# Optimization experiments

Measured on AMD Instinct MI355X. Metric: run time of the kernel, lower is better.

Reference implementation:

```python
import jax, jax.numpy as jnp
import numpy as np

D_MODEL = 1024
N_HEADS = 16
D_K = D_MODEL // N_HEADS
FF_DIM = 4096
EPS = 1e-6
NEG = -1.0e9


def _layernorm(x, g, b):
    # torch: a_2 * (x - mean) / (std + eps) + b_2, std is unbiased (ddof=1)
    mean = jnp.mean(x, axis=-1, keepdims=True)
    std = jnp.std(x, axis=-1, keepdims=True, ddof=1)
    return g * (x - mean) / (std + EPS) + b


def setup_inputs() -> dict:
    key = jax.random.key(0)
    ks = jax.random.split(key, 8)
    s = 0.02
    x = jax.random.normal(ks[0], (2, 2048, D_MODEL), dtype=jnp.float32)
    mask = jnp.ones((2, 1, 1, 2048), dtype=jnp.int32)
    return {
        "x": x,
        "mask": mask,
        "wq": jax.random.normal(ks[1], (D_MODEL, D_MODEL), jnp.float32) * s,
        "wk": jax.random.normal(ks[2], (D_MODEL, D_MODEL), jnp.float32) * s,
        "wv": jax.random.normal(ks[3], (D_MODEL, D_MODEL), jnp.float32) * s,
        "wo": jax.random.normal(ks[4], (D_MODEL, D_MODEL), jnp.float32) * s,
        "bq": jnp.zeros((D_MODEL,), jnp.float32),
        "bk": jnp.zeros((D_MODEL,), jnp.float32),
        "bv": jnp.zeros((D_MODEL,), jnp.float32),
        "bo": jnp.zeros((D_MODEL,), jnp.float32),
        "w1": jax.random.normal(ks[5], (D_MODEL, FF_DIM), jnp.float32) * s,
        "b1": jnp.zeros((FF_DIM,), jnp.float32),
        "w2": jax.random.normal(ks[6], (FF_DIM, D_MODEL), jnp.float32) * s,
        "b2": jnp.zeros((D_MODEL,), jnp.float32),
        "ln1_g": jnp.ones((D_MODEL,), jnp.float32),
        "ln1_b": jnp.zeros((D_MODEL,), jnp.float32),
        "ln2_g": jnp.ones((D_MODEL,), jnp.float32),
        "ln2_b": jnp.zeros((D_MODEL,), jnp.float32),
    }


def reference(x, mask, wq, wk, wv, wo, bq, bk, bv, bo, w1, b1, w2, b2,
              ln1_g, ln1_b, ln2_g, ln2_b):
    B, S, _ = x.shape
    # --- sublayer 1: pre-norm self-attention with residual ---
    h = _layernorm(x, ln1_g, ln1_b)
    q = (h @ wq + bq).reshape(B, S, N_HEADS, D_K).transpose(0, 2, 1, 3)
    k = (h @ wk + bk).reshape(B, S, N_HEADS, D_K).transpose(0, 2, 1, 3)
    v = (h @ wv + bv).reshape(B, S, N_HEADS, D_K).transpose(0, 2, 1, 3)
    scores = jnp.einsum('bhqd,bhkd->bhqk', q, k) / np.sqrt(D_K).astype(np.float32)
    scores = jnp.where(mask == 0, NEG, scores)
    attn = jax.nn.softmax(scores, axis=-1)
    ctx = jnp.einsum('bhqk,bhkd->bhqd', attn, v)
    ctx = ctx.transpose(0, 2, 1, 3).reshape(B, S, D_MODEL)
    x = x + (ctx @ wo + bo)
    # --- sublayer 2: pre-norm FFN with residual ---
    h2 = _layernorm(x, ln2_g, ln2_b)
    ff = jax.nn.relu(h2 @ w1 + b1) @ w2 + b2
    return x + ff
```

## Files before the change

### kernel.cpp

```cpp
#include <hip/hip_runtime.h>

typedef unsigned short u16;
typedef unsigned int u32;
typedef __attribute__((ext_vector_type(8))) short bf16x8;
typedef __attribute__((ext_vector_type(4))) float f32x4;

__device__ __forceinline__ u16 f2bf(float f) {
  union { float f; unsigned int u; } x;
  x.f = f;
  unsigned int r = x.u + 0x7fffu + ((x.u >> 16) & 1u);
  return (u16)(r >> 16);
}

__device__ __forceinline__ float bf2f(u16 v) {
  union { unsigned int u; float f; } x;
  x.u = ((unsigned int)v) << 16;
  return x.f;
}

__device__ __forceinline__ u32 fbits(float f) {
  union { float f; u32 u; } x; x.f = f; return x.u;
}

__device__ __forceinline__ void async16(const u16* g, u16* l) {
  __builtin_amdgcn_global_load_lds((const __attribute__((address_space(1))) void*)g,
                                   (__attribute__((address_space(3))) void*)l, 16, 0, 0);
}

__device__ __forceinline__ void stage128x64(const u16* __restrict__ src, long row0, int k0,
                                            int ld, u16* lds, int wave, int lane) {
#pragma unroll
  for (int r = 0; r < 4; ++r) {
    int s = r * 256 + wave * 64 + lane;
    int row = s >> 3;
    int c = (s & 7) ^ (row & 7);
    async16(src + (row0 + row) * (long)ld + k0 + c * 8, lds + (r * 256 + wave * 64) * 8);
  }
}

__device__ __forceinline__ void stage64x128(const u16* __restrict__ src, int col0, int ld,
                                            u16* lds, int wave, int lane) {
#pragma unroll
  for (int r = 0; r < 4; ++r) {
    int s = r * 256 + wave * 64 + lane;
    int row = s >> 4;
    int c = (s & 15) ^ (row & 15);
    async16(src + (long)row * ld + col0 + c * 8, lds + (r * 256 + wave * 64) * 8);
  }
}

__global__ __launch_bounds__(256) void transpose_cvt(const float* __restrict__ src,
                                                     u16* __restrict__ dst, int R, int C) {
  __shared__ float tile[32][33];
  int c0 = blockIdx.x * 32, r0 = blockIdx.y * 32;
  int tx = threadIdx.x & 31, ty = threadIdx.x >> 5;
#pragma unroll
  for (int i = 0; i < 32; i += 8)
    tile[ty + i][tx] = src[(long)(r0 + ty + i) * C + c0 + tx];
  __syncthreads();
#pragma unroll
  for (int i = 0; i < 32; i += 8)
    dst[(long)(c0 + ty + i) * R + r0 + tx] = f2bf(tile[tx][ty + i]);
}

__global__ __launch_bounds__(256) void transpose_cvt4(const float* __restrict__ s0,
                                                      const float* __restrict__ s1,
                                                      const float* __restrict__ s2,
                                                      const float* __restrict__ s3,
                                                      u16* __restrict__ dst) {
  __shared__ float tile[32][33];
  const float* src = blockIdx.z == 0 ? s0 : (blockIdx.z == 1 ? s1 : (blockIdx.z == 2 ? s2 : s3));
  u16* d = dst + (long)blockIdx.z * 1024 * 1024;
  int c0 = blockIdx.x * 32, r0 = blockIdx.y * 32;
  int tx = threadIdx.x & 31, ty = threadIdx.x >> 5;
#pragma unroll
  for (int i = 0; i < 32; i += 8)
    tile[ty + i][tx] = src[(long)(r0 + ty + i) * 1024 + c0 + tx];
  __syncthreads();
#pragma unroll
  for (int i = 0; i < 32; i += 8)
    d[(long)(c0 + ty + i) * 1024 + r0 + tx] = f2bf(tile[tx][ty + i]);
}

__device__ __forceinline__ void ln_core(float4 v, const float* g, const float* b, int t,
                                        u16* outrow) {
  float s = v.x + v.y + v.z + v.w;
  float ss = v.x * v.x + v.y * v.y + v.z * v.z + v.w * v.w;
#pragma unroll
  for (int off = 32; off; off >>= 1) {
    s += __shfl_xor(s, off);
    ss += __shfl_xor(ss, off);
  }
  __shared__ float red[8];
  int wave = t >> 6, lane = t & 63;
  if (lane == 0) { red[wave] = s; red[wave + 4] = ss; }
  __syncthreads();
  float tot = red[0] + red[1] + red[2] + red[3];
  float tots = red[4] + red[5] + red[6] + red[7];
  float mean = tot * (1.0f / 1024.0f);
  float var = (tots - 1024.0f * mean * mean) * (1.0f / 1023.0f);
  var = fmaxf(var, 0.0f);
  float inv = 1.0f / (sqrtf(var) + 1e-6f);
  float4 gv = ((const float4*)g)[t];
  float4 bv = ((const float4*)b)[t];
  union { unsigned long long u64; u16 h[4]; } o;
  o.h[0] = f2bf(gv.x * (v.x - mean) * inv + bv.x);
  o.h[1] = f2bf(gv.y * (v.y - mean) * inv + bv.y);
  o.h[2] = f2bf(gv.z * (v.z - mean) * inv + bv.z);
  o.h[3] = f2bf(gv.w * (v.w - mean) * inv + bv.w);
  *(unsigned long long*)(outrow + t * 4) = o.u64;
}

__global__ __launch_bounds__(256) void layernorm_rows(const float* __restrict__ x,
                                                      const float* __restrict__ g,
                                                      const float* __restrict__ b,
                                                      u16* __restrict__ out) {
  int row = blockIdx.x, t = threadIdx.x;
  float4 v = ((const float4*)(x + (long)row * 1024))[t];
  ln_core(v, g, b, t, out + (long)row * 1024);
}

__global__ __launch_bounds__(256) void ln_fuse(const float* __restrict__ x,
                                               const float* __restrict__ bres,
                                               const u16* __restrict__ p0,
                                               const u16* __restrict__ p1,
                                               const float* __restrict__ g,
                                               const float* __restrict__ b,
                                               float* __restrict__ yout,
                                               u16* __restrict__ hout) {
  int row = blockIdx.x, t = threadIdx.x;
  long base = (long)row * 1024;
  float4 xv = ((const float4*)(x + base))[t];
  float4 bo = ((const float4*)bres)[t];
  ushort4 a = ((const ushort4*)(p0 + base))[t];
  ushort4 c = ((const ushort4*)(p1 + base))[t];
  float4 y;
  y.x = xv.x + bo.x + bf2f(a.x) + bf2f(c.x);
  y.y = xv.y + bo.y + bf2f(a.y) + bf2f(c.y);
  y.z = xv.z + bo.z + bf2f(a.z) + bf2f(c.z);
  y.w = xv.w + bo.w + bf2f(a.w) + bf2f(c.w);
  ((float4*)(yout + base))[t] = y;
  ln_core(y, g, b, t, hout + base);
}

__global__ __launch_bounds__(256) void final_add(float* __restrict__ out,
                                                 const float* __restrict__ b2,
                                                 const u16* __restrict__ p0,
                                                 const u16* __restrict__ p1) {
  int row = blockIdx.x, t = threadIdx.x;
  long base = (long)row * 1024;
  float4 o = ((float4*)(out + base))[t];
  float4 bb = ((const float4*)b2)[t];
  ushort4 a = ((const ushort4*)(p0 + base))[t];
  ushort4 c = ((const ushort4*)(p1 + base))[t];
  o.x += bb.x + bf2f(a.x) + bf2f(c.x);
  o.y += bb.y + bf2f(a.y) + bf2f(c.y);
  o.z += bb.z + bf2f(a.z) + bf2f(c.z);
  o.w += bb.w + bf2f(a.w) + bf2f(c.w);
  ((float4*)(out + base))[t] = o;
}

template <int MODE>
__global__ __launch_bounds__(256) void gemm_bt(const u16* __restrict__ A,
                                               const u16* __restrict__ Bt, int M, int N, int K,
                                               void* __restrict__ outp,
                                               const float* __restrict__ bias0,
                                               const float* __restrict__ bias1,
                                               const float* __restrict__ bias2,
                                               u16* __restrict__ q_out, u16* __restrict__ k_out,
                                               u16* __restrict__ v_out) {
  __shared__ __align__(16) u16 lds[17408];
  u16* ldsA = lds;
  u16* ldsB = lds + 8192;
  const int tid = threadIdx.x;
  const int wave = tid >> 6, lane = tid & 63;
  const int lane16 = lane & 15, quad = lane >> 4;
  const int wm = (wave >> 1) * 64, wn = (wave & 1) * 64;
  const long m0 = (long)blockIdx.y * 128;
  const long n0 = (long)blockIdx.x * 128;
  const int kLen = K / gridDim.z;
  const int kBeg = blockIdx.z * kLen;

  const f32x4 fzero = {0.f, 0.f, 0.f, 0.f};
  f32x4 acc[4][4];
#pragma unroll
  for (int i = 0; i < 4; ++i)
#pragma unroll
    for (int j = 0; j < 4; ++j) acc[i][j] = fzero;

  for (int k0 = kBeg; k0 < kBeg + kLen; k0 += 64) {
    stage128x64(A, m0, k0, K, ldsA, wave, lane);
    stage128x64(Bt, n0, k0, K, ldsB, wave, lane);
    __syncthreads();
#pragma unroll
    for (int kk = 0; kk < 2; ++kk) {
      bf16x8 af[4], bfr[4];
#pragma unroll
      for (int i = 0; i < 4; ++i) {
        int row = wm + i * 16 + lane16;
        int c = (kk * 4 + quad) ^ (row & 7);
        af[i] = *(const bf16x8*)(ldsA + row * 64 + c * 8);
      }
#pragma unroll
      for (int j = 0; j < 4; ++j) {
        int row = wn + j * 16 + lane16;
        int c = (kk * 4 + quad) ^ (row & 7);
        bfr[j] = *(const bf16x8*)(ldsB + row * 64 + c * 8);
      }
#pragma unroll
      for (int i = 0; i < 4; ++i)
#pragma unroll
        for (int j = 0; j < 4; ++j)
          acc[i][j] = __builtin_amdgcn_mfma_f32_16x16x32_bf16(af[i], bfr[j], acc[i][j], 0, 0, 0);
    }
    __syncthreads();
  }

  if (MODE == 0 && (int)(n0 >> 10) == 2) {
#pragma unroll
    for (int j = 0; j < 4; ++j) {
      int lcol = wn + j * 16 + lane16;
      float bvj = bias2[(int)(n0 - 2048) + lcol];
#pragma unroll
      for (int i = 0; i < 4; ++i)
#pragma unroll
        for (int r = 0; r < 4; ++r) {
          int lrow = wm + i * 16 + quad * 4 + r;
          lds[lcol * 136 + lrow] = f2bf(acc[i][j][r] + bvj);
        }
    }
    __syncthreads();
    int lcol = tid >> 1, seg = tid & 1;
    int cc = (int)(n0 - 2048) + lcol;
    int head = cc >> 6, d = cc & 63;
    int bI = (int)(m0 >> 11), s0 = (int)(m0 & 2047);
    u16* dst = v_out + ((long)(bI * 16 + head) * 64 + d) * 2048 + s0 + seg * 64;
    const u16* s = lds + lcol * 136 + seg * 64;
#pragma unroll
    for (int c2 = 0; c2 < 8; ++c2) ((uint4*)dst)[c2] = ((const uint4*)s)[c2];
    return;
  }

  u16* pp = nullptr;
  if (MODE == 1) {
    pp = blockIdx.z == 0 ? (u16*)outp : (blockIdx.z == 1 ? q_out : (blockIdx.z == 2 ? k_out : v_out));
  }

#pragma unroll
  for (int j = 0; j < 4; ++j) {
    int col = (int)n0 + wn + j * 16 + lane16;
#pragma unroll
    for (int i = 0; i < 4; ++i) {
#pragma unroll
      for (int r = 0; r < 4; ++r) {
        int row = (int)m0 + wm + i * 16 + quad * 4 + r;
        float val = acc[i][j][r];
        if (MODE == 0) {
          int which = col >> 10, cc = col & 1023;
          float vv = val + (which == 0 ? bias0[cc] : bias1[cc]);
          int bb = row >> 11, sS = row & 2047, head = cc >> 6, d = cc & 63;
          long bh = (long)bb * 16 + head;
          if (which == 0) {
            q_out[(bh * 2048 + sS) * 64 + d] = f2bf(vv * 0.18033688f);
          } else {
            k_out[(bh * 2048 + sS) * 64 + d] = f2bf(vv);
          }
        } else if (MODE == 1) {
          pp[(long)row * N + col] = f2bf(val);
        } else if (MODE == 2) {
          ((u16*)outp)[(long)row * N + col] = f2bf(fmaxf(val + bias0[col], 0.0f));
        }
      }
    }
  }
}

#define FA_C0 28.854239f
__global__ __launch_bounds__(256) void flash_attn(const u16* __restrict__ q,
                                                  const u16* __restrict__ k,
                                                  const u16* __restrict__ v,
                                                  const int* __restrict__ mask,
                                                  u16* __restrict__ ctx) {
  const int bh = blockIdx.y;
  const int b = bh >> 4, h = bh & 15;
  const int q0 = blockIdx.x * 128;
  const int tid = threadIdx.x;
  const int wave = tid >> 6, lane = tid & 63;
  const int lane16 = lane & 15, quad = lane >> 4;

  const u16* qp = q + (long)bh * 2048 * 64;
  const u16* kp = k + (long)bh * 2048 * 64;
  const u16* vp = v + (long)bh * 64 * 2048;
  const int* mp = mask + b * 2048;

  __shared__ __align__(16) u16 ldsK[128 * 64];
  __shared__ __align__(16) u16 ldsVT[64 * 128];
  __shared__ __align__(16) u16 ldsP23[2 * 4096];
  __shared__ __align__(16) float ldsMask[128];
  __shared__ int ldsFlag[2];
  u16* myP = (wave < 2) ? (ldsK + wave * 4096) : (ldsP23 + (wave - 2) * 4096);

  bf16x8 qf[2][2];
#pragma unroll
  for (int g = 0; g < 2; ++g) {
    const long qrow = q0 + wave * 32 + g * 16 + lane16;
    qf[g][0] = *(const bf16x8*)(qp + qrow * 64 + quad * 8);
    qf[g][1] = *(const bf16x8*)(qp + qrow * 64 + 32 + quad * 8);
  }

  const f32x4 fzero = {0.f, 0.f, 0.f, 0.f};
  const f32x4 cC0 = {-FA_C0, -FA_C0, -FA_C0, -FA_C0};
  float l_loc[2] = {0.f, 0.f};
  f32x4 o_acc[2][4];
#pragma unroll
  for (int g = 0; g < 2; ++g)
#pragma unroll
    for (int j = 0; j < 4; ++j) o_acc[g][j] = fzero;

  const int xorm = (lane16 & 7) << 2;

  for (int kt = 0; kt < 2048; kt += 128) {
    stage128x64(kp, kt, 0, 64, ldsK, wave, lane);
    stage64x128(vp, kt, 2048, ldsVT, wave, lane);
    if (tid < 128) {
      int mv = mp[kt + tid];
      ldsMask[tid] = ((mv == 0) ? -1.0e9f : 0.0f) - FA_C0;
      unsigned long long bal = __ballot(mv != 0);
      if ((tid & 63) == 0) ldsFlag[tid >> 6] = (bal == ~0ull) ? 1 : 0;
    }
    __syncthreads();
    const bool allv = (ldsFlag[0] & ldsFlag[1]) != 0;

    f32x4 s_acc[8][2];
#pragma unroll
    for (int j = 0; j < 8; ++j) {
      f32x4 ci = allv ? cC0 : *(const f32x4*)(ldsMask + j * 16 + quad * 4);
      int row = j * 16 + lane16;
      int c0i = quad ^ (row & 7);
      int c1i = (4 + quad) ^ (row & 7);
      bf16x8 kf0 = *(const bf16x8*)(ldsK + row * 64 + c0i * 8);
      bf16x8 kf1 = *(const bf16x8*)(ldsK + row * 64 + c1i * 8);
#pragma unroll
      for (int g = 0; g < 2; ++g) {
        f32x4 sa = __builtin_amdgcn_mfma_f32_16x16x32_bf16(kf0, qf[g][0], ci, 0, 0, 0);
        sa = __builtin_amdgcn_mfma_f32_16x16x32_bf16(kf1, qf[g][1], sa, 0, 0, 0);
        s_acc[j][g] = sa;
      }
    }
    __syncthreads();

#pragma unroll
    for (int j = 0; j < 8; ++j) {
      int cw = (4 * j + quad) ^ xorm;
#pragma unroll
      for (int g = 0; g < 2; ++g) {
        float p0 = __builtin_exp2f(s_acc[j][g][0]);
        float p1 = __builtin_exp2f(s_acc[j][g][1]);
        float p2 = __builtin_exp2f(s_acc[j][g][2]);
        float p3 = __builtin_exp2f(s_acc[j][g][3]);
        l_loc[g] += (p0 + p1) + (p2 + p3);
        u32 lo = __builtin_amdgcn_perm(fbits(p1), fbits(p0), 0x07060302u);
        u32 hi = __builtin_amdgcn_perm(fbits(p3), fbits(p2), 0x07060302u);
        uint2 pk; pk.x = lo; pk.y = hi;
        *(uint2*)(myP + (g * 16 + lane16) * 128 + cw * 4) = pk;
      }
    }
#pragma unroll
    for (int kk = 0; kk < 4; ++kk) {
      int cr = (8 * kk + 2 * quad) ^ xorm;
      bf16x8 pf0 = *(const bf16x8*)(myP + lane16 * 128 + cr * 4);
      bf16x8 pf1 = *(const bf16x8*)(myP + (16 + lane16) * 128 + cr * 4);
#pragma unroll
      for (int jj = 0; jj < 4; ++jj) {
        int row = jj * 16 + lane16;
        int cv = (kk * 4 + quad) ^ (row & 15);
        bf16x8 vf = *(const bf16x8*)(ldsVT + row * 128 + cv * 8);
        o_acc[0][jj] = __builtin_amdgcn_mfma_f32_16x16x32_bf16(pf0, vf, o_acc[0][jj], 0, 0, 0);
        o_acc[1][jj] = __builtin_amdgcn_mfma_f32_16x16x32_bf16(pf1, vf, o_acc[1][jj], 0, 0, 0);
      }
    }
    __syncthreads();
  }

  float lr[2][4];
#pragma unroll
  for (int g = 0; g < 2; ++g) {
    float l = l_loc[g];
#pragma unroll
    for (int off = 16; off < 64; off <<= 1) l += __shfl_xor(l, off);
    float linv = 1.0f / l;
#pragma unroll
    for (int r = 0; r < 4; ++r) lr[g][r] = __shfl(linv, quad * 4 + r);
  }

#pragma unroll
  for (int g = 0; g < 2; ++g)
#pragma unroll
    for (int jj = 0; jj < 4; ++jj)
#pragma unroll
      for (int r = 0; r < 4; ++r) {
        int sg = q0 + wave * 32 + g * 16 + quad * 4 + r;
        int d = jj * 16 + lane16;
        float val = o_acc[g][jj][r] * lr[g][r];
        ctx[((long)b * 2048 + sg) * 1024 + h * 64 + d] = f2bf(val);
      }
}

extern "C" void kernel_launch(void* const* d_in, const int* in_sizes, int n_in, void* d_out,
                              int out_size, void* d_ws, size_t ws_size, hipStream_t stream) {
  (void)in_sizes; (void)n_in; (void)out_size; (void)ws_size;
  const float* x  = (const float*)d_in[0];
  const int* mask = (const int*)d_in[1];
  const float* wq = (const float*)d_in[2];
  const float* wk = (const float*)d_in[3];
  const float* wv = (const float*)d_in[4];
  const float* wo = (const float*)d_in[5];
  const float* bq = (const float*)d_in[6];
  const float* bk = (const float*)d_in[7];
  const float* bv = (const float*)d_in[8];
  const float* bo = (const float*)d_in[9];
  const float* w1 = (const float*)d_in[10];
  const float* b1 = (const float*)d_in[11];
  const float* w2 = (const float*)d_in[12];
  const float* b2 = (const float*)d_in[13];
  const float* ln1_g = (const float*)d_in[14];
  const float* ln1_b = (const float*)d_in[15];
  const float* ln2_g = (const float*)d_in[16];
  const float* ln2_b = (const float*)d_in[17];
  float* out = (float*)d_out;

  u16* ws = (u16*)d_ws;
  u16* wqkvT = ws;
  u16* woT = wqkvT + 3072 * 1024;
  u16* w1T = woT + 1024 * 1024;
  u16* w2T = w1T + 4096 * 1024;
  u16* h   = w2T + 4096 * 1024;
  u16* qb  = h + 4096 * 1024;
  u16* kb  = qb + 4096 * 1024;
  u16* vb  = kb + 4096 * 1024;
  u16* ctx = vb + 4096 * 1024;
  u16* ffh = qb;
  u16* f2p0 = ws;
  u16* f2p1 = w1T;

  transpose_cvt4<<<dim3(32, 32, 4), 256, 0, stream>>>(wq, wk, wv, wo, wqkvT);
  transpose_cvt<<<dim3(128, 32), 256, 0, stream>>>(w1, w1T, 1024, 4096);
  transpose_cvt<<<dim3(32, 128), 256, 0, stream>>>(w2, w2T, 4096, 1024);

  layernorm_rows<<<4096, 256, 0, stream>>>(x, ln1_g, ln1_b, h);

  gemm_bt<0><<<dim3(24, 32), 256, 0, stream>>>(h, wqkvT, 4096, 3072, 1024, nullptr, bq, bk, bv,
                                               qb, kb, vb);

  flash_attn<<<dim3(16, 32), 256, 0, stream>>>(qb, kb, vb, mask, ctx);

  gemm_bt<1><<<dim3(8, 32, 2), 256, 0, stream>>>(ctx, woT, 4096, 1024, 1024, qb, nullptr,
                                                 nullptr, nullptr, kb, nullptr, nullptr);

  ln_fuse<<<4096, 256, 0, stream>>>(x, bo, qb, kb, ln2_g, ln2_b, out, h);

  gemm_bt<2><<<dim3(32, 32), 256, 0, stream>>>(h, w1T, 4096, 4096, 1024, ffh, b1, nullptr,
                                               nullptr, nullptr, nullptr, nullptr);

  gemm_bt<1><<<dim3(8, 32, 2), 256, 0, stream>>>(ffh, w2T, 4096, 1024, 4096, f2p0, nullptr,
                                                 nullptr, nullptr, f2p1, nullptr, nullptr);

  final_add<<<4096, 256, 0, stream>>>(out, b2, f2p0, f2p1);
}
```

Baseline: 376.7 us.

## Merge weight prep and layernorm into one launch; fuse softmax into QK loop

The three weight transpose/convert kernels and the first layernorm are folded into a single prep kernel that dispatches on block index, so four launches become one and their tails can overlap. In flash attention, P now has a dedicated LDS buffer per wave instead of reusing the K buffer for two waves. That lets exp2 and the P write happen straight after each QK MFMA without the intermediate score array or the extra barrier. The mask add is applied only when a tile is not fully valid, and the end-of-loop barrier moves to the start of the next iteration. The cost is more LDS per block, which may lower occupancy, and the mask offset constant is now always folded into the MFMA initial accumulator.

```diff
diff --git a/kernel.cpp b/kernel.cpp
--- a/kernel.cpp
+++ b/kernel.cpp
@@ -47,39 +47,6 @@
     int c = (s & 15) ^ (row & 15);
     async16(src + (long)row * ld + col0 + c * 8, lds + (r * 256 + wave * 64) * 8);
   }
-}
-
-__global__ __launch_bounds__(256) void transpose_cvt(const float* __restrict__ src,
-                                                     u16* __restrict__ dst, int R, int C) {
-  __shared__ float tile[32][33];
-  int c0 = blockIdx.x * 32, r0 = blockIdx.y * 32;
-  int tx = threadIdx.x & 31, ty = threadIdx.x >> 5;
-#pragma unroll
-  for (int i = 0; i < 32; i += 8)
-    tile[ty + i][tx] = src[(long)(r0 + ty + i) * C + c0 + tx];
-  __syncthreads();
-#pragma unroll
-  for (int i = 0; i < 32; i += 8)
-    dst[(long)(c0 + ty + i) * R + r0 + tx] = f2bf(tile[tx][ty + i]);
-}
-
-__global__ __launch_bounds__(256) void transpose_cvt4(const float* __restrict__ s0,
-                                                      const float* __restrict__ s1,
-                                                      const float* __restrict__ s2,
-                                                      const float* __restrict__ s3,
-                                                      u16* __restrict__ dst) {
-  __shared__ float tile[32][33];
-  const float* src = blockIdx.z == 0 ? s0 : (blockIdx.z == 1 ? s1 : (blockIdx.z == 2 ? s2 : s3));
-  u16* d = dst + (long)blockIdx.z * 1024 * 1024;
-  int c0 = blockIdx.x * 32, r0 = blockIdx.y * 32;
-  int tx = threadIdx.x & 31, ty = threadIdx.x >> 5;
-#pragma unroll
-  for (int i = 0; i < 32; i += 8)
-    tile[ty + i][tx] = src[(long)(r0 + ty + i) * 1024 + c0 + tx];
-  __syncthreads();
-#pragma unroll
-  for (int i = 0; i < 32; i += 8)
-    d[(long)(c0 + ty + i) * 1024 + r0 + tx] = f2bf(tile[tx][ty + i]);
 }
 
 __device__ __forceinline__ void ln_core(float4 v, const float* g, const float* b, int t,
@@ -111,13 +78,49 @@
   *(unsigned long long*)(outrow + t * 4) = o.u64;
 }
 
-__global__ __launch_bounds__(256) void layernorm_rows(const float* __restrict__ x,
-                                                      const float* __restrict__ g,
-                                                      const float* __restrict__ b,
-                                                      u16* __restrict__ out) {
-  int row = blockIdx.x, t = threadIdx.x;
-  float4 v = ((const float4*)(x + (long)row * 1024))[t];
-  ln_core(v, g, b, t, out + (long)row * 1024);
+__global__ __launch_bounds__(256) void prep(const float* __restrict__ wq,
+                                            const float* __restrict__ wk,
+                                            const float* __restrict__ wv,
+                                            const float* __restrict__ wo,
+                                            const float* __restrict__ w1,
+                                            const float* __restrict__ w2,
+                                            const float* __restrict__ x,
+                                            const float* __restrict__ ln1_g,
+                                            const float* __restrict__ ln1_b,
+                                            u16* __restrict__ wqkvT,
+                                            u16* __restrict__ w1T,
+                                            u16* __restrict__ w2T,
+                                            u16* __restrict__ hout) {
+  const int bid = blockIdx.x;
+  const int part = bid >> 12;
+  const int local = bid & 4095;
+  const int t = threadIdx.x;
+  if (part == 1) {
+    float4 v = ((const float4*)(x + (long)local * 1024))[t];
+    ln_core(v, ln1_g, ln1_b, t, hout + (long)local * 1024);
+    return;
+  }
+  __shared__ float tile[32][33];
+  const float* src; u16* dst; int C, R, bx, by;
+  if (part == 0) {
+    int sub = local >> 10;
+    src = sub == 0 ? wq : (sub == 1 ? wk : (sub == 2 ? wv : wo));
+    dst = wqkvT + (long)sub * 1024 * 1024;
+    C = 1024; R = 1024; bx = local & 31; by = (local >> 5) & 31;
+  } else if (part == 2) {
+    src = w1; dst = w1T; C = 4096; R = 1024; bx = local & 127; by = local >> 7;
+  } else {
+    src = w2; dst = w2T; C = 1024; R = 4096; bx = local & 31; by = local >> 5;
+  }
+  int c0 = bx * 32, r0 = by * 32;
+  int tx = t & 31, ty = t >> 5;
+#pragma unroll
+  for (int i = 0; i < 32; i += 8)
+    tile[ty + i][tx] = src[(long)(r0 + ty + i) * C + c0 + tx];
+  __syncthreads();
+#pragma unroll
+  for (int i = 0; i < 32; i += 8)
+    dst[(long)(c0 + ty + i) * R + r0 + tx] = f2bf(tile[tx][ty + i]);
 }
 
 __global__ __launch_bounds__(256) void ln_fuse(const float* __restrict__ x,
@@ -242,9 +245,7 @@
   }
 
   u16* pp = nullptr;
-  if (MODE == 1) {
-    pp = blockIdx.z == 0 ? (u16*)outp : (blockIdx.z == 1 ? q_out : (blockIdx.z == 2 ? k_out : v_out));
-  }
+  if (MODE == 1) pp = blockIdx.z == 0 ? (u16*)outp : q_out;
 
 #pragma unroll
   for (int j = 0; j < 4; ++j) {
@@ -295,10 +296,10 @@
 
   __shared__ __align__(16) u16 ldsK[128 * 64];
   __shared__ __align__(16) u16 ldsVT[64 * 128];
-  __shared__ __align__(16) u16 ldsP23[2 * 4096];
+  __shared__ __align__(16) u16 ldsP[4 * 4096];
   __shared__ __align__(16) float ldsMask[128];
   __shared__ int ldsFlag[2];
-  u16* myP = (wave < 2) ? (ldsK + wave * 4096) : (ldsP23 + (wave - 2) * 4096);
+  u16* myP = ldsP + wave * 4096;
 
   bf16x8 qf[2][2];
 #pragma unroll
@@ -318,58 +319,54 @@
     for (int j = 0; j < 4; ++j) o_acc[g][j] = fzero;
 
   const int xorm = (lane16 & 7) << 2;
+  u16* const pw0 = myP + lane16 * 128;
+  u16* const pw1 = myP + (16 + lane16) * 128;
 
   for (int kt = 0; kt < 2048; kt += 128) {
+    if (kt) __syncthreads();
     stage128x64(kp, kt, 0, 64, ldsK, wave, lane);
     stage64x128(vp, kt, 2048, ldsVT, wave, lane);
     if (tid < 128) {
       int mv = mp[kt + tid];
-      ldsMask[tid] = ((mv == 0) ? -1.0e9f : 0.0f) - FA_C0;
+      ldsMask[tid] = (mv == 0) ? -1.0e9f : 0.0f;
       unsigned long long bal = __ballot(mv != 0);
       if ((tid & 63) == 0) ldsFlag[tid >> 6] = (bal == ~0ull) ? 1 : 0;
     }
     __syncthreads();
     const bool allv = (ldsFlag[0] & ldsFlag[1]) != 0;
 
-    f32x4 s_acc[8][2];
 #pragma unroll
     for (int j = 0; j < 8; ++j) {
-      f32x4 ci = allv ? cC0 : *(const f32x4*)(ldsMask + j * 16 + quad * 4);
       int row = j * 16 + lane16;
       int c0i = quad ^ (row & 7);
       int c1i = (4 + quad) ^ (row & 7);
       bf16x8 kf0 = *(const bf16x8*)(ldsK + row * 64 + c0i * 8);
       bf16x8 kf1 = *(const bf16x8*)(ldsK + row * 64 + c1i * 8);
+      int cw = ((4 * j + quad) ^ xorm) * 4;
 #pragma unroll
       for (int g = 0; g < 2; ++g) {
-        f32x4 sa = __builtin_amdgcn_mfma_f32_16x16x32_bf16(kf0, qf[g][0], ci, 0, 0, 0);
+        f32x4 sa = __builtin_amdgcn_mfma_f32_16x16x32_bf16(kf0, qf[g][0], cC0, 0, 0, 0);
         sa = __builtin_amdgcn_mfma_f32_16x16x32_bf16(kf1, qf[g][1], sa, 0, 0, 0);
-        s_acc[j][g] = sa;
-      }
-    }
-    __syncthreads();
-
-#pragma unroll
-    for (int j = 0; j < 8; ++j) {
-      int cw = (4 * j + quad) ^ xorm;
-#pragma unroll
-      for (int g = 0; g < 2; ++g) {
-        float p0 = __builtin_exp2f(s_acc[j][g][0]);
-        float p1 = __builtin_exp2f(s_acc[j][g][1]);
-        float p2 = __builtin_exp2f(s_acc[j][g][2]);
-        float p3 = __builtin_exp2f(s_acc[j][g][3]);
+        if (!allv) {
+          f32x4 mk = *(const f32x4*)(ldsMask + j * 16 + quad * 4);
+          sa = sa + mk;
+        }
+        float p0 = __builtin_exp2f(sa[0]);
+        float p1 = __builtin_exp2f(sa[1]);
+        float p2 = __builtin_exp2f(sa[2]);
+        float p3 = __builtin_exp2f(sa[3]);
         l_loc[g] += (p0 + p1) + (p2 + p3);
-        u32 lo = __builtin_amdgcn_perm(fbits(p1), fbits(p0), 0x07060302u);
-        u32 hi = __builtin_amdgcn_perm(fbits(p3), fbits(p2), 0x07060302u);
-        uint2 pk; pk.x = lo; pk.y = hi;
-        *(uint2*)(myP + (g * 16 + lane16) * 128 + cw * 4) = pk;
+        uint2 pk;
+        pk.x = __builtin_amdgcn_perm(fbits(p1), fbits(p0), 0x07060302u);
+        pk.y = __builtin_amdgcn_perm(fbits(p3), fbits(p2), 0x07060302u);
+        *(uint2*)((g ? pw1 : pw0) + cw) = pk;
       }
     }
 #pragma unroll
     for (int kk = 0; kk < 4; ++kk) {
-      int cr = (8 * kk + 2 * quad) ^ xorm;
-      bf16x8 pf0 = *(const bf16x8*)(myP + lane16 * 128 + cr * 4);
-      bf16x8 pf1 = *(const bf16x8*)(myP + (16 + lane16) * 128 + cr * 4);
+      int cr = ((8 * kk + 2 * quad) ^ xorm) * 4;
+      bf16x8 pf0 = *(const bf16x8*)(pw0 + cr);
+      bf16x8 pf1 = *(const bf16x8*)(pw1 + cr);
 #pragma unroll
       for (int jj = 0; jj < 4; ++jj) {
         int row = jj * 16 + lane16;
@@ -379,7 +376,6 @@
         o_acc[1][jj] = __builtin_amdgcn_mfma_f32_16x16x32_bf16(pf1, vf, o_acc[1][jj], 0, 0, 0);
       }
     }
-    __syncthreads();
   }
 
   float lr[2][4];
@@ -443,11 +439,8 @@
   u16* f2p0 = ws;
   u16* f2p1 = w1T;
 
-  transpose_cvt4<<<dim3(32, 32, 4), 256, 0, stream>>>(wq, wk, wv, wo, wqkvT);
-  transpose_cvt<<<dim3(128, 32), 256, 0, stream>>>(w1, w1T, 1024, 4096);
-  transpose_cvt<<<dim3(32, 128), 256, 0, stream>>>(w2, w2T, 4096, 1024);
-
-  layernorm_rows<<<4096, 256, 0, stream>>>(x, ln1_g, ln1_b, h);
+  prep<<<16384, 256, 0, stream>>>(wq, wk, wv, wo, w1, w2, x, ln1_g, ln1_b,
+                                  wqkvT, w1T, w2T, h);
 
   gemm_bt<0><<<dim3(24, 32), 256, 0, stream>>>(h, wqkvT, 4096, 3072, 1024, nullptr, bq, bk, bv,
                                                qb, kb, vb);
```

After: 370.0 us. No clear change (-1.8%).
